# Performance work log

Hardware: AMD Instinct MI355X
Metric: run time of the kernel (lower is better)

The kernel has to match this reference:

```python
import jax, jax.numpy as jnp
import numpy as np

UNITS = 32      # 12 inter + 19 command + 1 motor
SENSORY = 32    # dense_2 output dim
MOTOR = 1
ODE_UNFOLDS = 6
EPS = 1e-8


def _build_wiring():
    # kerasncp NCP wiring: motor ids [0,1), command [1,20), inter [20,32)
    rng = np.random.RandomState(42)
    inter = np.arange(20, 32)
    command = np.arange(1, 20)
    motor = np.arange(0, 1)
    adj = np.zeros((UNITS, UNITS), np.float32)
    sens = np.zeros((SENSORY, UNITS), np.float32)
    for s in range(SENSORY):                      # sensory_fanout=6 onto inter neurons
        for d in rng.choice(inter, 6, replace=False):
            sens[s, d] = rng.choice([-1.0, 1.0])
    for i in inter:                               # inter_fanout=4 onto command neurons
        for d in rng.choice(command, 4, replace=False):
            adj[i, d] = rng.choice([-1.0, 1.0])
    for _ in range(6):                            # 6 recurrent command synapses
        adj[rng.choice(command), rng.choice(command)] = rng.choice([-1.0, 1.0])
    for m in motor:                               # motor_fanin=4 from command neurons
        for srcn in rng.choice(command, 4, replace=False):
            adj[srcn, m] = rng.choice([-1.0, 1.0])
    return adj, sens


def setup_inputs() -> dict:
    key = jax.random.key(0)
    ks = jax.random.split(key, 12)
    B, T = 256, 1024
    adj, sens = _build_wiring()
    u = lambda k, sh, lo, hi: jax.random.uniform(k, sh, jnp.float32, lo, hi)
    return {
        "x": jax.random.normal(ks[0], (B, T, 2), jnp.float32),
        "d1_w": jax.random.normal(ks[1], (2, 128), jnp.float32) * (1.0 / np.sqrt(2.0)),
        "d1_b": jnp.zeros((128,), jnp.float32),
        "d2_w": jax.random.normal(ks[2], (128, SENSORY), jnp.float32) * (1.0 / np.sqrt(128.0)),
        "d2_b": jnp.zeros((SENSORY,), jnp.float32),
        "input_w": jnp.ones((SENSORY,), jnp.float32),
        "input_b": jnp.zeros((SENSORY,), jnp.float32),
        "output_w": jnp.ones((MOTOR,), jnp.float32),
        "output_b": jnp.zeros((MOTOR,), jnp.float32),
        "gleak": u(ks[3], (UNITS,), 0.001, 1.0),
        "vleak": u(ks[4], (UNITS,), -0.2, 0.2),
        "cm": u(ks[5], (UNITS,), 0.4, 0.6),
        "w_syn": u(ks[6], (UNITS, UNITS), 0.001, 1.0),
        "mu": u(ks[7], (UNITS, UNITS), 0.3, 0.8),
        "sigma": u(ks[8], (UNITS, UNITS), 3.0, 8.0),
        "erev": jnp.asarray(adj),
        "sensory_w": u(ks[9], (SENSORY, UNITS), 0.001, 1.0),
        "sensory_mu": u(ks[10], (SENSORY, UNITS), 0.3, 0.8),
        "sensory_sigma": u(ks[11], (SENSORY, UNITS), 3.0, 8.0),
        "sensory_erev": jnp.asarray(sens),
        "sparsity_mask": jnp.asarray(np.abs(adj), jnp.int32),
        "sensory_mask": jnp.asarray(np.abs(sens), jnp.int32),
    }


def reference(x, d1_w, d1_b, d2_w, d2_b, input_w, input_b, output_w, output_b,
              gleak, vleak, cm, w_syn, mu, sigma, erev,
              sensory_w, sensory_mu, sensory_sigma, sensory_erev,
              sparsity_mask, sensory_mask):
    # Dense stack (per timestep)
    h = jax.nn.relu(x @ d1_w + d1_b)          # [B,T,128]
    h = h @ d2_w + d2_b                        # [B,T,32] sensory inputs
    spm = sparsity_mask.astype(h.dtype)
    ssm = sensory_mask.astype(h.dtype)

    def gate(v, m, s):                         # v [B,pre] -> [B,pre,post]
        return jax.nn.sigmoid(s * (v[..., None] - m))

    cm_t = cm * ODE_UNFOLDS                    # cm / (elapsed_time / ode_unfolds), elapsed_time=1

    def step(v, xt):
        inp = xt * input_w + input_b           # LTC input mapping (affine)
        sa = sensory_w * gate(inp, sensory_mu, sensory_sigma) * ssm   # [B,32,32]
        wnum_s = jnp.sum(sa * sensory_erev, axis=1)                   # [B,32]
        wden_s = jnp.sum(sa, axis=1)

        def unfold(vp, _):
            wa = w_syn * gate(vp, mu, sigma) * spm                    # [B,32,32]
            wnum = jnp.sum(wa * erev, axis=1) + wnum_s
            wden = jnp.sum(wa, axis=1) + wden_s
            vp = (cm_t * vp + gleak * vleak + wnum) / (cm_t + gleak + wden + EPS)
            return vp, None

        v, _ = jax.lax.scan(unfold, v, None, length=ODE_UNFOLDS)
        return v, None

    v0 = jnp.zeros((h.shape[0], UNITS), h.dtype)
    vT, _ = jax.lax.scan(step, v0, jnp.swapaxes(h, 0, 1))  # scan over T
    # output mapping: motor neurons are the first MOTOR states
    return vT[:, :MOTOR] * output_w + output_b             # [B,1]
```

## Files before the change

kernel.cpp:

```cpp
#include <hip/hip_runtime.h>
#include <math.h>

#define NB 256
#define NT 1024
#define NUNF 6
#define TB 64
#define CHK 8
#define L2E 1.44269504088896340736f
#define PI_F 3.14159265358979324f

typedef const float* fp;

extern "C" __device__ float __ocml_exp2_f32(float);
__device__ __forceinline__ float frcp(float x) { return __builtin_amdgcn_rcpf(x); }
__device__ __forceinline__ float ex2(float x) { return __ocml_exp2_f32(x); }
__device__ __forceinline__ float sgm(float a, float b, float v) { return frcp(1.f + ex2(fmaf(a, v, b))); }

struct Tables {
    int ngroups, npos, nchunks, pad0;
    int grp_start[21];
    int ord[20];
    int pos[20];
    int aff[20];
    int need_traj[20];
    int ch_ps[20], ch_pe[20], ch_gs[20], ch_ge[20];
    int ncp[20], nip[20], ngp[20];
    float cmt[20], cn0[20], cd0[20];
    float icmt[12];
    int   cp_pre[20][8];
    float cp_a[20][8], cp_b[20][8], cp_w[20][8], cp_e[20][8];
    int   ip_i[20][12];
    float ip_a[20][12], ip_b[20][12], ip_w[20][12], ip_e[20][12];
    int   gp_pre[20][6];
    float gp_a[20][6], gp_b[20][6], gp_w[20][6], gp_e[20][6];
};

struct DenseTab {
    int cnt[12];
    float in0[12], id0[12];
    int   pre[12][32];
    float a[12][32], b[12][32], w[12][32], e[12][32];
    int homog, maxcnt;
};

#define WS_DTAB   16384
#define WS_BND    24576
#define WS_BMASK  25600
#define WS_MG     32768
#define WS_VST    98304
#define WS_SENSI  131072

__global__ void build_tables(fp wsyn, fp mu, fp sigma, fp erev, const int* spm,
                             fp sw, fp smu, fp ssg, fp serev, const int* smask,
                             fp cm, fp gleak, fp vleak, fp d1b, Tables* T, DenseTab* D) {
    __shared__ int   spmL[1024], smkL[1024];
    __shared__ float wL[1024], muL[1024], sgL[1024], evL[1024];
    __shared__ float swL[1024], smuL[1024], ssgL[1024], sevL[1024];
    __shared__ float cmL[32], glL[32], vlL[32];
    __shared__ int premaskL[20], ancL[20], rootL[20], depUL[20], keyL[20], posL[20], ordL[20];
    __shared__ int ngpL[20];
    __shared__ int neededS;
    __shared__ float habs[64];
    __shared__ int cntS[12];
    int tid = threadIdx.x;
    for (int k = tid; k < 1024; k += 64) {
        spmL[k] = spm[k]; wL[k] = wsyn[k]; muL[k] = mu[k]; sgL[k] = sigma[k]; evL[k] = erev[k];
        smkL[k] = smask[k]; swL[k] = sw[k]; smuL[k] = smu[k]; ssgL[k] = ssg[k]; sevL[k] = serev[k];
    }
    if (tid < 32) { cmL[tid] = cm[tid]; glL[tid] = gleak[tid]; vlL[tid] = vleak[tid]; }
    habs[tid] = fmaxf(fabsf(d1b[tid]), fabsf(d1b[tid + 64]));
    __syncthreads();
    if (tid < 20) {
        int pm = 0;
        for (int i = 0; i < 20; ++i) if (spmL[i * 32 + tid]) pm |= 1 << i;
        premaskL[tid] = pm;
        ancL[tid] = pm;
    }
    __syncthreads();
    for (int it = 0; it < 20; ++it) {
        int a = 0;
        if (tid < 20) {
            a = ancL[tid];
            int pm = premaskL[tid];
            for (int i = 0; i < 20; ++i) if ((pm >> i) & 1) a |= ancL[i];
        }
        __syncthreads();
        if (tid < 20) ancL[tid] = a;
        __syncthreads();
    }
    if (tid == 0) neededS = ancL[0] | 1;
    __syncthreads();
    int needed = neededS;
    if (tid < 20) {
        int r = tid;
        if ((needed >> tid) & 1) {
            int aj = ancL[tid];
            for (int i = 0; i < 20; ++i)
                if (i < r && ((needed >> i) & 1) && ((aj >> i) & 1) && ((ancL[i] >> tid) & 1)) r = i;
        }
        rootL[tid] = r;
        depUL[tid] = 0;
    }
    __syncthreads();
    for (int it = 0; it < 21; ++it) {
        int d = 0;
        if (tid < 20 && ((needed >> tid) & 1)) {
            int pm = premaskL[tid], myr = rootL[tid];
            for (int i = 0; i < 20; ++i)
                if (((pm >> i) & 1) && rootL[i] != myr) d = max(d, depUL[i] + 1);
        }
        __syncthreads();
        if (tid < 20 && d > depUL[tid]) depUL[tid] = d;
        __syncthreads();
    }
    if (tid < 20) {
        int key = 0x7FFFFFFF;
        if ((needed >> tid) & 1) {
            int myr = rootL[tid], dg = 0;
            for (int i = 0; i < 20; ++i)
                if (((needed >> i) & 1) && rootL[i] == myr) dg = max(dg, depUL[i]);
            key = dg * 32 + myr;
        }
        keyL[tid] = key;
    }
    __syncthreads();
    if (tid < 20) {
        int mykey = keyL[tid];
        int p = 0;
        for (int k = 0; k < 20; ++k)
            if (keyL[k] < mykey || (keyL[k] == mykey && k < tid)) ++p;
        posL[tid] = p;
        if (p < 20) ordL[p] = tid;
    }
    __syncthreads();
    if (tid < 20) {
        int j = tid, cc = 0, ci = 0, cg = 0;
        T->cmt[j] = cmL[j] * (float)NUNF;
        T->cn0[j] = glL[j] * vlL[j];
        T->cd0[j] = cmL[j] * (float)NUNF + glL[j] + 1e-8f;
        if ((needed >> j) & 1) {
            int myr = rootL[j];
            int mystart = posL[myr];
            for (int i = 0; i < 32; ++i) {
                int p = i * 32 + j;
                if (!spmL[p]) continue;
                float sg = sgL[p];
                float a = -sg * L2E, b = sg * muL[p] * L2E;
                float w = wL[p], e = w * evL[p];
                if (i >= 20) {
                    T->ip_i[j][ci] = i - 20;
                    T->ip_a[j][ci] = a; T->ip_b[j][ci] = b; T->ip_w[j][ci] = w; T->ip_e[j][ci] = e;
                    ++ci;
                } else if (rootL[i] == myr) {
                    T->gp_pre[j][cg] = posL[i] - mystart;
                    T->gp_a[j][cg] = a; T->gp_b[j][cg] = b; T->gp_w[j][cg] = w; T->gp_e[j][cg] = e;
                    ++cg;
                } else {
                    T->cp_pre[j][cc] = posL[i];
                    T->cp_a[j][cc] = a; T->cp_b[j][cc] = b; T->cp_w[j][cc] = w; T->cp_e[j][cc] = e;
                    ++cc;
                }
            }
        }
        T->ncp[j] = cc; T->nip[j] = ci; T->ngp[j] = cg;
        ngpL[j] = cg;
    }
    if (tid < 12) {
        T->icmt[tid] = cmL[20 + tid] * (float)NUNF;
        int unit = 20 + tid, cnt = 0;
        for (int s = 0; s < 32; ++s) {
            int p = s * 32 + unit;
            if (!smkL[p]) continue;
            float sg = ssgL[p];
            D->pre[tid][cnt] = s;
            D->a[tid][cnt] = -sg * L2E;
            D->b[tid][cnt] = sg * smuL[p] * L2E;
            D->w[tid][cnt] = swL[p];
            D->e[tid][cnt] = swL[p] * sevL[p];
            ++cnt;
        }
        for (int c = cnt; c < 32; ++c) {
            D->pre[tid][c] = 0; D->a[tid][c] = 0.f; D->b[tid][c] = 0.f;
            D->w[tid][c] = 0.f; D->e[tid][c] = 0.f;
        }
        D->cnt[tid] = cnt;
        cntS[tid] = cnt;
        D->in0[tid] = glL[unit] * vlL[unit];
        D->id0[tid] = cmL[unit] * (float)NUNF + glL[unit] + 1e-8f;
    }
    __syncthreads();
    if (tid == 0) {
        int npos = __popc(needed & 0xFFFFF);
        T->npos = npos;
        int ng = 0, prevkey = -1;
        for (int p = 0; p < npos; ++p) {
            int u = ordL[p];
            if (keyL[u] != prevkey) { T->grp_start[ng] = p; ++ng; prevkey = keyL[u]; }
        }
        T->ngroups = ng;
        for (int g = ng; g <= 20; ++g) T->grp_start[g] = npos;
        for (int p = 0; p < 20; ++p) T->ord[p] = (p < npos) ? ordL[p] : 0;
        for (int j = 0; j < 20; ++j) T->pos[j] = posL[j];
        for (int g = 0; g < ng; ++g) {
            int gs = T->grp_start[g], ge = T->grp_start[g + 1], gsz = ge - gs;
            for (int p = gs; p < ge; ++p)
                T->aff[p] = (gsz == 1 && ngpL[ordL[p]] == 0) ? 1 : 0;
        }
        for (int p = npos; p < 20; ++p) T->aff[p] = 0;
        for (int p = 0; p < 20; ++p) T->need_traj[p] = 0;
        for (int i = 0; i < 20; ++i) {
            if (!((needed >> i) & 1)) continue;
            for (int j = 0; j < 20; ++j)
                if (j != i && ((needed >> j) & 1) && spmL[i * 32 + j]) { T->need_traj[posL[i]] = 1; break; }
        }
        int nchunks = 0, g = 0;
        while (g < ng) {
            int lvl = keyL[ordL[T->grp_start[g]]] / 32;
            int ge = g;
            while (ge < ng && keyL[ordL[T->grp_start[ge]]] / 32 == lvl) ++ge;
            int cs = g;
            while (cs < ge) {
                int ce = cs, acc = 0;
                while (ce < ge) {
                    int gsz = T->grp_start[ce + 1] - T->grp_start[ce];
                    if (acc + gsz > CHK && ce > cs) break;
                    acc += gsz; ++ce;
                    if (acc >= CHK) break;
                }
                T->ch_gs[nchunks] = cs; T->ch_ge[nchunks] = ce;
                T->ch_ps[nchunks] = T->grp_start[cs]; T->ch_pe[nchunks] = T->grp_start[ce];
                ++nchunks;
                cs = ce;
            }
            g = ge;
        }
        T->nchunks = nchunks;
        float hm = 0.f;
        for (int k = 0; k < 64; ++k) hm = fmaxf(hm, habs[k]);
        D->homog = (hm == 0.f) ? 1 : 0;
        int mc = 0;
        for (int k = 0; k < 12; ++k) mc = max(mc, cntS[k]);
        D->maxcnt = mc;
    }
}

__global__ void sector_prep(fp d1w, float* bnd, int* bmask) {
    __shared__ float ang[256];
    __shared__ float uS[128], vS[128];
    int tid = threadIdx.x;
    if (tid < 128) { uS[tid] = d1w[tid]; vS[tid] = d1w[128 + tid]; }
    __syncthreads();
    {
        int k = tid & 127;
        float al = atan2f(vS[k], uS[k]);
        float bb = (tid < 128) ? al + 1.57079632679489662f : al - 1.57079632679489662f;
        if (bb > PI_F) bb -= 2.f * PI_F;
        if (bb <= -PI_F) bb += 2.f * PI_F;
        ang[tid] = bb;
    }
    __syncthreads();
    for (int k = 2; k <= 256; k <<= 1) {
        for (int j = k >> 1; j > 0; j >>= 1) {
            int ixj = tid ^ j;
            if (ixj > tid) {
                float a0 = ang[tid], a1 = ang[ixj];
                bool up = ((tid & k) == 0);
                if ((a0 > a1) == up) { ang[tid] = a1; ang[ixj] = a0; }
            }
            __syncthreads();
        }
    }
    bnd[tid] = ang[tid];
    float lo = ang[tid];
    float hi = (tid < 255) ? ang[tid + 1] : ang[0] + 2.f * PI_F;
    float tm = 0.5f * (lo + hi);
    float ct = cosf(tm), st = sinf(tm);
    for (int w = 0; w < 4; ++w) {
        int m = 0;
        for (int kk = 0; kk < 32; ++kk) {
            int k = w * 32 + kk;
            if (fmaf(uS[k], ct, vS[k] * st) > 0.f) m |= 1 << kk;
        }
        bmask[tid * 4 + w] = m;
    }
}

__global__ void sector_M(fp d1w, fp d2w, fp iw, const int* bmask, float2* Mg) {
    int s = blockIdx.x, j = threadIdx.x;
    if (j >= 32) return;
    float acc0 = 0.f, acc1 = 0.f;
#pragma unroll
    for (int w = 0; w < 4; ++w) {
        int mm = bmask[s * 4 + w];
        for (int kk = 0; kk < 32; ++kk) {
            if ((mm >> kk) & 1) {
                int k = w * 32 + kk;
                float w2 = d2w[k * 32 + j];
                acc0 = fmaf(d1w[k], w2, acc0);
                acc1 = fmaf(d1w[128 + k], w2, acc1);
            }
        }
    }
    float iwj = iw[j];
    Mg[s * 32 + j] = make_float2(acc0 * iwj, acc1 * iwj);
}

__global__ __launch_bounds__(256) void dense_homog(
    fp x, fp d2b, fp iw, fp ib,
    const DenseTab* __restrict__ Dg, const float2* __restrict__ Mg, const float* __restrict__ bndg,
    float2* sensI, int t0, int CT) {
    if (Dg->homog == 0) return;
    __shared__ float bndL[256];
    __shared__ float4 tabT[416];
    __shared__ int   preT[416];
    __shared__ float ibuf[4][2112];
    __shared__ float b2q[32], iwq[32], ibq[32];
    __shared__ float in0L[12], id0L[12];
    int tid = threadIdx.x;
    for (int idx = tid; idx < 384; idx += 256) {
        int d = idx >> 5, e = idx & 31;
        int sl = e * 13 + d;
        tabT[sl] = make_float4(Dg->a[d][e], Dg->b[d][e], Dg->w[d][e], Dg->e[d][e]);
        preT[sl] = Dg->pre[d][e];
    }
    if (tid < 12) { in0L[tid] = Dg->in0[tid]; id0L[tid] = Dg->id0[tid]; }
    if (tid < 32) { b2q[tid] = d2b[tid]; iwq[tid] = iw[tid]; ibq[tid] = ib[tid]; }
    if (tid < 256) bndL[tid] = bndg[tid];
    __syncthreads();
    int wid = tid >> 6, lane = tid & 63;
    const float2* x2 = (const float2*)x;
    int gw = blockIdx.x * 4 + wid;
    int nw = gridDim.x * 4;
    float* ibf = ibuf[wid];
    int jj = lane & 31, h = lane >> 5;
    float cj = fmaf(b2q[jj], iwq[jj], ibq[jj]);
    int cntmax = Dg->maxcnt;
    int pass_total = (NB * CT) >> 6;
    for (int pass = gw; pass < pass_total; pass += nw) {
        int cg0 = pass * 64;
        int cg = cg0 + lane;
        int lt = cg >> 8, bb_ = cg & 255;
        float2 xv = x2[bb_ * NT + (t0 + lt)];
        float th = atan2f(xv.y, xv.x);
        int sec;
        if (th < bndL[0]) sec = 255;
        else {
            int lo = 0, hi = 255;
#pragma unroll
            for (int it7 = 0; it7 < 8; ++it7) {
                int mid = (lo + hi + 1) >> 1;
                if (bndL[mid] <= th) lo = mid; else hi = mid - 1;
            }
            sec = lo;
        }
        float x0r = xv.x, x1r = xv.y;
#pragma unroll 4
        for (int r = 0; r < 32; ++r) {
            int item = 2 * r + h;
            int s_it = __shfl(sec, item);
            float xi0 = __shfl(x0r, item);
            float xi1 = __shfl(x1r, item);
            float2 m = Mg[s_it * 32 + jj];
            ibf[item * 33 + jj] = fmaf(xi0, m.x, fmaf(xi1, m.y, cj));
        }
        __builtin_amdgcn_wave_barrier();
#pragma unroll
        for (int rb = 0; rb < 12; ++rb) {
            int task = rb * 64 + lane;
            int item = task / 12;
            int dd = task - item * 12;
            float wn = in0L[dd], wd = id0L[dd];
            for (int e = 0; e < cntmax; ++e) {
                int sl = e * 13 + dd;
                float4 tb = tabT[sl];
                float pv = ibf[item * 33 + preT[sl]];
                float gq = frcp(1.f + ex2(fmaf(tb.x, pv, tb.y)));
                wn = fmaf(tb.w, gq, wn);
                wd = fmaf(tb.z, gq, wd);
            }
            int cg2 = cg0 + item;
            int lt2 = cg2 >> 8, b2_ = cg2 & 255;
            sensI[(size_t)(b2_ * CT + lt2) * 12 + dd] = make_float2(wn, wd);
        }
        __builtin_amdgcn_wave_barrier();
    }
}

__global__ __launch_bounds__(256) void dense_general(
    fp x, fp d1w, fp d1b, fp d2w, fp d2b, fp iw, fp ib,
    const DenseTab* __restrict__ Dg, float2* sensI, int t0, int CT) {
    if (Dg->homog != 0) return;
    __shared__ float W2s[4096];
    __shared__ float W1s[256], b1s[128];
    __shared__ float b2q[32], iwq[32], ibq[32];
    __shared__ float4 tabT[416];
    __shared__ int   preT[416];
    __shared__ int   cntL[12];
    __shared__ float in0L[12], id0L[12];
    __shared__ float hbuf[4][128][20];
    __shared__ float ibuf[4][16][33];
    int tid = threadIdx.x;
    for (int idx = tid; idx < 384; idx += 256) {
        int d = idx >> 5, e = idx & 31;
        int sl = e * 13 + d;
        tabT[sl] = make_float4(Dg->a[d][e], Dg->b[d][e], Dg->w[d][e], Dg->e[d][e]);
        preT[sl] = Dg->pre[d][e];
    }
    if (tid < 12) { cntL[tid] = Dg->cnt[tid]; in0L[tid] = Dg->in0[tid]; id0L[tid] = Dg->id0[tid]; }
    for (int p = tid; p < 4096; p += 256) W2s[p] = d2w[p];
    if (tid < 256) W1s[tid] = d1w[tid];
    if (tid < 128) b1s[tid] = d1b[tid];
    if (tid < 32) { b2q[tid] = d2b[tid]; iwq[tid] = iw[tid]; ibq[tid] = ib[tid]; }
    __syncthreads();
    int wid = tid >> 6, lane = tid & 63;
    float* hb = (float*)hbuf[wid];
    float* ibf = (float*)ibuf[wid];
    const float2* x2 = (const float2*)x;
    int gw = blockIdx.x * 4 + wid;
    int nw = gridDim.x * 4;
    int pass_total = (NB * CT) >> 4;
    int itd1 = lane >> 2, kq = lane & 3;
    int j = lane & 31, half = lane >> 5;
    for (int pass = gw; pass < pass_total; pass += nw) {
        int cg0 = pass * 16;
        {
            int cg = cg0 + itd1;
            int lt = cg >> 8, b = cg & 255;
            float2 xv = x2[b * NT + (t0 + lt)];
#pragma unroll 8
            for (int i = 0; i < 32; ++i) {
                int k = kq + 4 * i;
                float hk = fmaf(xv.y, W1s[128 + k], fmaf(xv.x, W1s[k], b1s[k]));
                hb[k * 20 + itd1] = hk > 0.f ? hk : 0.f;
            }
        }
        __builtin_amdgcn_wave_barrier();
        {
            float a0=0,a1=0,a2=0,a3=0,a4=0,a5=0,a6=0,a7=0;
#pragma unroll 4
            for (int k = 0; k < 128; ++k) {
                float w2 = W2s[k * 32 + j];
                float4 ha = *(const float4*)&hb[k * 20 + half * 8];
                float4 hbv = *(const float4*)&hb[k * 20 + half * 8 + 4];
                a0 = fmaf(ha.x, w2, a0); a1 = fmaf(ha.y, w2, a1);
                a2 = fmaf(ha.z, w2, a2); a3 = fmaf(ha.w, w2, a3);
                a4 = fmaf(hbv.x, w2, a4); a5 = fmaf(hbv.y, w2, a5);
                a6 = fmaf(hbv.z, w2, a6); a7 = fmaf(hbv.w, w2, a7);
            }
            float bb = b2q[j], iww = iwq[j], ibb = ibq[j];
            ibf[(half*8+0)*33+j] = fmaf(a0+bb, iww, ibb);
            ibf[(half*8+1)*33+j] = fmaf(a1+bb, iww, ibb);
            ibf[(half*8+2)*33+j] = fmaf(a2+bb, iww, ibb);
            ibf[(half*8+3)*33+j] = fmaf(a3+bb, iww, ibb);
            ibf[(half*8+4)*33+j] = fmaf(a4+bb, iww, ibb);
            ibf[(half*8+5)*33+j] = fmaf(a5+bb, iww, ibb);
            ibf[(half*8+6)*33+j] = fmaf(a6+bb, iww, ibb);
            ibf[(half*8+7)*33+j] = fmaf(a7+bb, iww, ibb);
        }
        __builtin_amdgcn_wave_barrier();
#pragma unroll
        for (int r = 0; r < 3; ++r) {
            int task = r * 64 + lane;
            int it = task / 12;
            int d = task - it * 12;
            int cnt = cntL[d];
            float wn = in0L[d], wd = id0L[d];
            for (int e = 0; e < cnt; ++e) {
                int sl = e * 13 + d;
                float4 tb = tabT[sl];
                float gq = frcp(1.f + ex2(fmaf(tb.x, ibf[it * 33 + preT[sl]], tb.y)));
                wn = fmaf(tb.w, gq, wn);
                wd = fmaf(tb.z, gq, wd);
            }
            int cg = cg0 + it;
            int lt = cg >> 8, b = cg & 255;
            sensI[(size_t)(b * CT + lt) * 12 + d] = make_float2(wn, wd);
        }
        __builtin_amdgcn_wave_barrier();
    }
}

__global__ __launch_bounds__(512) void solve(const float2* __restrict__ sensI,
                                             const Tables* __restrict__ Tg,
                                             fp ow, fp ob, float* vstate,
                                             int t0, int CT, float* out) {
    __shared__ Tables TL;
    __shared__ float2 iAB[TB * 12];
    __shared__ float2 icomp[TB * 12];
    __shared__ float viter[TB * 13];
    __shared__ float vtraj[20 * TB * 7];
    __shared__ float2 pnpd[CHK * TB * 7];
    __shared__ float2 comp[CHK * TB];
    __shared__ float vstart[CHK * TB];
    __shared__ float gstate[20], istate[12];
    int tid = threadIdx.x;
    int b = blockIdx.x;
    {
        const int nw = (int)(sizeof(Tables) / 4);
        const int* src = (const int*)Tg;
        int* dst = (int*)&TL;
        for (int k = tid; k < nw; k += 512) dst[k] = src[k];
    }
    __syncthreads();
    if (tid < 20 && tid < TL.npos)
        gstate[tid] = (t0 == 0) ? 0.f : vstate[b * 32 + TL.ord[tid]];
    if (tid < 12)
        istate[tid] = (t0 == 0) ? 0.f : vstate[b * 32 + 20 + tid];
    __syncthreads();
    int ntiles = CT / TB;
    bool lastChunk = (t0 + CT == NT);
    for (int tile = 0; tile < ntiles; ++tile) {
        int tbase = tile * TB;
        for (int w = tid; w < TB * 16; w += 512) {
            int tt = w >> 4, ii = w & 15;
            if (ii < 12) {
                float2 s = sensI[(size_t)(b * CT + tbase + tt) * 12 + ii];
                float r = frcp(s.y);
                float A = TL.icmt[ii] * r, B = s.x * r;
                iAB[tt * 12 + ii] = make_float2(A, B);
                float A2 = A * A, A4 = A2 * A2;
                float A6 = A4 * A2;
                float B6 = B * (1.f + A) * (1.f + A2 + A4);
                icomp[tt * 12 + ii] = make_float2(A6, B6);
            }
        }
        __syncthreads();
        if (tid < 12) {
            float v = istate[tid];
#pragma unroll 4
            for (int tt = 0; tt < TB; ++tt) {
                viter[tt * 13 + tid] = v;
                float2 cc = icomp[tt * 12 + tid];
                v = fmaf(cc.x, v, cc.y);
            }
            istate[tid] = v;
        }
        __syncthreads();
        int nchunks = TL.nchunks;
        for (int c = 0; c < nchunks; ++c) {
            int ps = TL.ch_ps[c], pe = TL.ch_pe[c];
            int gs0 = TL.ch_gs[c], ge0 = TL.ch_ge[c];
            int npc = pe - ps;
            for (int w = tid; w < npc * TB; w += 512) {
                int m = w >> 6, tt = w & (TB - 1);
                int posi = ps + m;
                int unit = TL.ord[posi];
                float pn[6], pd[6];
#pragma unroll
                for (int u = 0; u < 6; ++u) { pn[u] = TL.cn0[unit]; pd[u] = TL.cd0[unit]; }
                int ncp = TL.ncp[unit];
                for (int e = 0; e < ncp; ++e) {
                    int pp = TL.cp_pre[unit][e];
                    float a = TL.cp_a[unit][e], bb = TL.cp_b[unit][e];
                    float w_ = TL.cp_w[unit][e], ev = TL.cp_e[unit][e];
#pragma unroll
                    for (int u = 0; u < 6; ++u) {
                        float gq = sgm(a, bb, vtraj[(pp * TB + tt) * 7 + u]);
                        pn[u] = fmaf(ev, gq, pn[u]);
                        pd[u] = fmaf(w_, gq, pd[u]);
                    }
                }
                int nip = TL.nip[unit];
                for (int e = 0; e < nip; ++e) {
                    int ii = TL.ip_i[unit][e];
                    float2 ab = iAB[tt * 12 + ii];
                    float vi = viter[tt * 13 + ii];
                    float a = TL.ip_a[unit][e], bb = TL.ip_b[unit][e];
                    float w_ = TL.ip_w[unit][e], ev = TL.ip_e[unit][e];
#pragma unroll
                    for (int u = 0; u < 6; ++u) {
                        float gq = sgm(a, bb, vi);
                        pn[u] = fmaf(ev, gq, pn[u]);
                        pd[u] = fmaf(w_, gq, pd[u]);
                        vi = fmaf(ab.x, vi, ab.y);
                    }
                }
                if (TL.aff[posi]) {
                    float cmt = TL.cmt[unit];
                    float Ac = 1.f, Bc = 0.f;
#pragma unroll
                    for (int u = 0; u < 6; ++u) {
                        float r = frcp(pd[u]);
                        float Au = cmt * r, Bu = pn[u] * r;
                        pnpd[(m * TB + tt) * 7 + u] = make_float2(Au, Bu);
                        Bc = fmaf(Au, Bc, Bu);
                        Ac *= Au;
                    }
                    comp[m * TB + tt] = make_float2(Ac, Bc);
                } else {
#pragma unroll
                    for (int u = 0; u < 6; ++u)
                        pnpd[(m * TB + tt) * 7 + u] = make_float2(pn[u], pd[u]);
                }
            }
            __syncthreads();
            if (tid < ge0 - gs0) {
                int g = gs0 + tid;
                int gs = TL.grp_start[g], ge = TL.grp_start[g + 1], gsz = ge - gs;
                int m0 = gs - ps;
                if (gsz == 1) {
                    int unit = TL.ord[gs];
                    float v = gstate[gs];
                    if (TL.aff[gs]) {
#pragma unroll 4
                        for (int tt = 0; tt < TB; ++tt) {
                            vstart[m0 * TB + tt] = v;
                            float2 cc = comp[m0 * TB + tt];
                            v = fmaf(cc.x, v, cc.y);
                        }
                    } else {
                        float ga = TL.gp_a[unit][0], gb = TL.gp_b[unit][0];
                        float gw = TL.gp_w[unit][0], gev = TL.gp_e[unit][0];
                        float cmt = TL.cmt[unit];
                        int ntj = TL.need_traj[gs];
                        for (int tt = 0; tt < TB; ++tt) {
#pragma unroll
                            for (int u = 0; u < 6; ++u) {
                                if (ntj) vtraj[(gs * TB + tt) * 7 + u] = v;
                                float2 pp2 = pnpd[(m0 * TB + tt) * 7 + u];
                                float E = ex2(fmaf(ga, v, gb));
                                float P = fmaf(cmt, v, pp2.x);
                                float N = fmaf(P, E, P + gev);
                                float Dd = fmaf(pp2.y, E, pp2.y + gw);
                                v = N * frcp(Dd);
                            }
                        }
                    }
                    gstate[gs] = v;
                } else {
                    float sv[CHK], nv[CHK];
#pragma unroll
                    for (int mm = 0; mm < CHK; ++mm) if (mm < gsz) sv[mm] = gstate[gs + mm];
                    for (int tt = 0; tt < TB; ++tt) {
#pragma unroll
                        for (int u = 0; u < 6; ++u) {
#pragma unroll
                            for (int mm = 0; mm < CHK; ++mm)
                                if (mm < gsz) vtraj[((gs + mm) * TB + tt) * 7 + u] = sv[mm];
#pragma unroll
                            for (int mm = 0; mm < CHK; ++mm) {
                                if (mm < gsz) {
                                    int unit = TL.ord[gs + mm];
                                    float2 pp2 = pnpd[((m0 + mm) * TB + tt) * 7 + u];
                                    float wn = pp2.x, wd = pp2.y;
                                    int ngpu = TL.ngp[unit];
#pragma unroll
                                    for (int e = 0; e < 6; ++e) {
                                        if (e < ngpu) {
                                            float vp = sv[TL.gp_pre[unit][e]];
                                            float gq = sgm(TL.gp_a[unit][e], TL.gp_b[unit][e], vp);
                                            wn = fmaf(TL.gp_e[unit][e], gq, wn);
                                            wd = fmaf(TL.gp_w[unit][e], gq, wd);
                                        }
                                    }
                                    nv[mm] = fmaf(TL.cmt[unit], sv[mm], wn) * frcp(wd);
                                }
                            }
#pragma unroll
                            for (int mm = 0; mm < CHK; ++mm) if (mm < gsz) sv[mm] = nv[mm];
                        }
                    }
#pragma unroll
                    for (int mm = 0; mm < CHK; ++mm) if (mm < gsz) gstate[gs + mm] = sv[mm];
                }
            }
            __syncthreads();
            for (int w = tid; w < npc * TB; w += 512) {
                int m = w >> 6, tt = w & (TB - 1);
                int posi = ps + m;
                if (TL.aff[posi] && TL.need_traj[posi]) {
                    float v = vstart[m * TB + tt];
#pragma unroll
                    for (int u = 0; u < 6; ++u) {
                        vtraj[(posi * TB + tt) * 7 + u] = v;
                        float2 ab = pnpd[(m * TB + tt) * 7 + u];
                        v = fmaf(ab.x, v, ab.y);
                    }
                }
            }
            __syncthreads();
        }
    }
    if (tid < 20 && tid < TL.npos) vstate[b * 32 + TL.ord[tid]] = gstate[tid];
    if (tid < 12) vstate[b * 32 + 20 + tid] = istate[tid];
    if (lastChunk) {
        __syncthreads();
        if (tid == 0) out[b] = fmaf(gstate[TL.pos[0]], ow[0], ob[0]);
    }
}

extern "C" void kernel_launch(void* const* d_in, const int* in_sizes, int n_in,
                              void* d_out, int out_size, void* d_ws, size_t ws_size,
                              hipStream_t stream) {
    fp x     = (fp)d_in[0];
    fp d1w   = (fp)d_in[1];
    fp d1b   = (fp)d_in[2];
    fp d2w   = (fp)d_in[3];
    fp d2b   = (fp)d_in[4];
    fp iw    = (fp)d_in[5];
    fp ib    = (fp)d_in[6];
    fp ow    = (fp)d_in[7];
    fp ob    = (fp)d_in[8];
    fp gleak = (fp)d_in[9];
    fp vleak = (fp)d_in[10];
    fp cm    = (fp)d_in[11];
    fp wsyn  = (fp)d_in[12];
    fp mu    = (fp)d_in[13];
    fp sigma = (fp)d_in[14];
    fp erev  = (fp)d_in[15];
    fp sw    = (fp)d_in[16];
    fp smu   = (fp)d_in[17];
    fp ssg   = (fp)d_in[18];
    fp serev = (fp)d_in[19];
    const int* spm   = (const int*)d_in[20];
    const int* smask = (const int*)d_in[21];

    char* wsb = (char*)d_ws;
    Tables*   T = (Tables*)wsb;
    DenseTab* D = (DenseTab*)(wsb + WS_DTAB);
    float*   bnd = (float*)(wsb + WS_BND);
    int*   bmask = (int*)(wsb + WS_BMASK);
    float2*   Mg = (float2*)(wsb + WS_MG);
    float* vstate = (float*)(wsb + WS_VST);
    float2* sensI = (float2*)(wsb + WS_SENSI);

    size_t per_t = (size_t)NB * 12 * sizeof(float2);
    int CT = TB;
    if (ws_size > WS_SENSI) {
        size_t m = (ws_size - WS_SENSI) / per_t;
        int ct = TB;
        while (ct < NT && (size_t)(ct * 2) <= m) ct *= 2;
        CT = ct;
    }

    build_tables<<<1, 64, 0, stream>>>(wsyn, mu, sigma, erev, spm,
                                       sw, smu, ssg, serev, smask,
                                       cm, gleak, vleak, d1b, T, D);
    sector_prep<<<1, 256, 0, stream>>>(d1w, bnd, bmask);
    sector_M<<<256, 64, 0, stream>>>(d1w, d2w, iw, bmask, Mg);

    int nch = NT / CT;
    for (int c = 0; c < nch; ++c) {
        int t0 = c * CT;
        dense_homog<<<768, 256, 0, stream>>>(x, d2b, iw, ib, D, Mg, bnd, sensI, t0, CT);
        dense_general<<<512, 256, 0, stream>>>(x, d1w, d1b, d2w, d2b, iw, ib, D, sensI, t0, CT);
        solve<<<NB, 512, 0, stream>>>(sensI, T, ow, ob, vstate, t0, CT, (float*)d_out);
    }
}
```

Measured before the change: 298.1 us.

## Double solve time tile via compacted trajectory slots and on-the-fly inter compose

Doubles the solve kernel's time tile from 64 to 128 steps, which halves the number of tile iterations and their barriers per block. To fit in shared memory, trajectory storage is compacted so only command neurons that feed others get a slot, with indices remapped in the tables. The precomputed icomp buffer is removed and the inter-neuron sixth-power composition is now computed inside the serial 12-thread loop. The larger shared footprint may reduce occupancy, and the serial inter loop does more arithmetic per step.

```diff
diff --git a/kernel.cpp b/kernel.cpp
--- a/kernel.cpp
+++ b/kernel.cpp
@@ -4,8 +4,9 @@
 #define NB 256
 #define NT 1024
 #define NUNF 6
-#define TB 64
+#define TBS 128
 #define CHK 8
+#define NTJMAX 12
 #define L2E 1.44269504088896340736f
 #define PI_F 3.14159265358979324f
 
@@ -17,12 +18,13 @@
 __device__ __forceinline__ float sgm(float a, float b, float v) { return frcp(1.f + ex2(fmaf(a, v, b))); }
 
 struct Tables {
-    int ngroups, npos, nchunks, pad0;
+    int ngroups, npos, nchunks, ntraj;
     int grp_start[21];
     int ord[20];
     int pos[20];
     int aff[20];
     int need_traj[20];
+    int traj_slot[20];
     int ch_ps[20], ch_pe[20], ch_gs[20], ch_ge[20];
     int ncp[20], nip[20], ngp[20];
     float cmt[20], cn0[20], cd0[20];
@@ -58,7 +60,7 @@
     __shared__ float swL[1024], smuL[1024], ssgL[1024], sevL[1024];
     __shared__ float cmL[32], glL[32], vlL[32];
     __shared__ int premaskL[20], ancL[20], rootL[20], depUL[20], keyL[20], posL[20], ordL[20];
-    __shared__ int ngpL[20];
+    __shared__ int ngpL[20], ntjL[20], slotU[20];
     __shared__ int neededS;
     __shared__ float habs[64];
     __shared__ int cntS[12];
@@ -131,6 +133,20 @@
             if (keyL[k] < mykey || (keyL[k] == mykey && k < tid)) ++p;
         posL[tid] = p;
         if (p < 20) ordL[p] = tid;
+    }
+    __syncthreads();
+    if (tid < 20) {
+        int nt = 0;
+        if ((needed >> tid) & 1)
+            for (int j = 0; j < 20; ++j)
+                if (j != tid && ((needed >> j) & 1) && spmL[tid * 32 + j]) { nt = 1; break; }
+        ntjL[tid] = nt;
+    }
+    __syncthreads();
+    if (tid == 0) {
+        int s = 0;
+        for (int p = 0; p < 20; ++p) { int u = ordL[p]; slotU[u] = s; s += ntjL[u]; }
+        T->ntraj = s;
     }
     __syncthreads();
     if (tid < 20) {
@@ -156,7 +172,7 @@
                     T->gp_a[j][cg] = a; T->gp_b[j][cg] = b; T->gp_w[j][cg] = w; T->gp_e[j][cg] = e;
                     ++cg;
                 } else {
-                    T->cp_pre[j][cc] = posL[i];
+                    T->cp_pre[j][cc] = slotU[i];
                     T->cp_a[j][cc] = a; T->cp_b[j][cc] = b; T->cp_w[j][cc] = w; T->cp_e[j][cc] = e;
                     ++cc;
                 }
@@ -207,11 +223,10 @@
                 T->aff[p] = (gsz == 1 && ngpL[ordL[p]] == 0) ? 1 : 0;
         }
         for (int p = npos; p < 20; ++p) T->aff[p] = 0;
-        for (int p = 0; p < 20; ++p) T->need_traj[p] = 0;
-        for (int i = 0; i < 20; ++i) {
-            if (!((needed >> i) & 1)) continue;
-            for (int j = 0; j < 20; ++j)
-                if (j != i && ((needed >> j) & 1) && spmL[i * 32 + j]) { T->need_traj[posL[i]] = 1; break; }
+        for (int p = 0; p < 20; ++p) {
+            int u = ordL[p];
+            T->need_traj[p] = ntjL[u];
+            T->traj_slot[p] = slotU[u];
         }
         int nchunks = 0, g = 0;
         while (g < ng) {
@@ -485,13 +500,12 @@
                                              fp ow, fp ob, float* vstate,
                                              int t0, int CT, float* out) {
     __shared__ Tables TL;
-    __shared__ float2 iAB[TB * 12];
-    __shared__ float2 icomp[TB * 12];
-    __shared__ float viter[TB * 13];
-    __shared__ float vtraj[20 * TB * 7];
-    __shared__ float2 pnpd[CHK * TB * 7];
-    __shared__ float2 comp[CHK * TB];
-    __shared__ float vstart[CHK * TB];
+    __shared__ float2 iAB[TBS * 12];
+    __shared__ float viter[TBS * 13];
+    __shared__ float vtraj[NTJMAX * TBS * 7];
+    __shared__ float2 pnpd[CHK * TBS * 7];
+    __shared__ float2 comp[CHK * TBS];
+    __shared__ float vstart[CHK * TBS];
     __shared__ float gstate[20], istate[12];
     int tid = threadIdx.x;
     int b = blockIdx.x;
@@ -507,31 +521,30 @@
     if (tid < 12)
         istate[tid] = (t0 == 0) ? 0.f : vstate[b * 32 + 20 + tid];
     __syncthreads();
-    int ntiles = CT / TB;
+    int ntiles = CT / TBS;
     bool lastChunk = (t0 + CT == NT);
     for (int tile = 0; tile < ntiles; ++tile) {
-        int tbase = tile * TB;
-        for (int w = tid; w < TB * 16; w += 512) {
+        int tbase = tile * TBS;
+        for (int w = tid; w < TBS * 16; w += 512) {
             int tt = w >> 4, ii = w & 15;
             if (ii < 12) {
                 float2 s = sensI[(size_t)(b * CT + tbase + tt) * 12 + ii];
                 float r = frcp(s.y);
-                float A = TL.icmt[ii] * r, B = s.x * r;
-                iAB[tt * 12 + ii] = make_float2(A, B);
-                float A2 = A * A, A4 = A2 * A2;
-                float A6 = A4 * A2;
-                float B6 = B * (1.f + A) * (1.f + A2 + A4);
-                icomp[tt * 12 + ii] = make_float2(A6, B6);
+                iAB[tt * 12 + ii] = make_float2(TL.icmt[ii] * r, s.x * r);
             }
         }
         __syncthreads();
         if (tid < 12) {
             float v = istate[tid];
 #pragma unroll 4
-            for (int tt = 0; tt < TB; ++tt) {
+            for (int tt = 0; tt < TBS; ++tt) {
+                float2 ab = iAB[tt * 12 + tid];
+                float A = ab.x, B = ab.y;
+                float A2 = A * A, A4 = A2 * A2;
+                float A6 = A4 * A2;
+                float B6 = B * (1.f + A) * (1.f + A2 + A4);
                 viter[tt * 13 + tid] = v;
-                float2 cc = icomp[tt * 12 + tid];
-                v = fmaf(cc.x, v, cc.y);
+                v = fmaf(A6, v, B6);
             }
             istate[tid] = v;
         }
@@ -541,8 +554,8 @@
             int ps = TL.ch_ps[c], pe = TL.ch_pe[c];
             int gs0 = TL.ch_gs[c], ge0 = TL.ch_ge[c];
             int npc = pe - ps;
-            for (int w = tid; w < npc * TB; w += 512) {
-                int m = w >> 6, tt = w & (TB - 1);
+            for (int w = tid; w < npc * TBS; w += 512) {
+                int m = w >> 7, tt = w & (TBS - 1);
                 int posi = ps + m;
                 int unit = TL.ord[posi];
                 float pn[6], pd[6];
@@ -550,12 +563,12 @@
                 for (int u = 0; u < 6; ++u) { pn[u] = TL.cn0[unit]; pd[u] = TL.cd0[unit]; }
                 int ncp = TL.ncp[unit];
                 for (int e = 0; e < ncp; ++e) {
-                    int pp = TL.cp_pre[unit][e];
+                    int sl = TL.cp_pre[unit][e];
                     float a = TL.cp_a[unit][e], bb = TL.cp_b[unit][e];
                     float w_ = TL.cp_w[unit][e], ev = TL.cp_e[unit][e];
 #pragma unroll
                     for (int u = 0; u < 6; ++u) {
-                        float gq = sgm(a, bb, vtraj[(pp * TB + tt) * 7 + u]);
+                        float gq = sgm(a, bb, vtraj[(sl * TBS + tt) * 7 + u]);
                         pn[u] = fmaf(ev, gq, pn[u]);
                         pd[u] = fmaf(w_, gq, pd[u]);
                     }
@@ -582,15 +595,15 @@
                     for (int u = 0; u < 6; ++u) {
                         float r = frcp(pd[u]);
                         float Au = cmt * r, Bu = pn[u] * r;
-                        pnpd[(m * TB + tt) * 7 + u] = make_float2(Au, Bu);
+                        pnpd[(m * TBS + tt) * 7 + u] = make_float2(Au, Bu);
                         Bc = fmaf(Au, Bc, Bu);
                         Ac *= Au;
                     }
-                    comp[m * TB + tt] = make_float2(Ac, Bc);
+                    comp[m * TBS + tt] = make_float2(Ac, Bc);
                 } else {
 #pragma unroll
                     for (int u = 0; u < 6; ++u)
-                        pnpd[(m * TB + tt) * 7 + u] = make_float2(pn[u], pd[u]);
+                        pnpd[(m * TBS + tt) * 7 + u] = make_float2(pn[u], pd[u]);
                 }
             }
             __syncthreads();
@@ -603,9 +616,9 @@
                     float v = gstate[gs];
                     if (TL.aff[gs]) {
 #pragma unroll 4
-                        for (int tt = 0; tt < TB; ++tt) {
-                            vstart[m0 * TB + tt] = v;
-                            float2 cc = comp[m0 * TB + tt];
+                        for (int tt = 0; tt < TBS; ++tt) {
+                            vstart[m0 * TBS + tt] = v;
+                            float2 cc = comp[m0 * TBS + tt];
                             v = fmaf(cc.x, v, cc.y);
                         }
                     } else {
@@ -613,11 +626,12 @@
                         float gw = TL.gp_w[unit][0], gev = TL.gp_e[unit][0];
                         float cmt = TL.cmt[unit];
                         int ntj = TL.need_traj[gs];
-                        for (int tt = 0; tt < TB; ++tt) {
+                        int sl = TL.traj_slot[gs];
+                        for (int tt = 0; tt < TBS; ++tt) {
 #pragma unroll
                             for (int u = 0; u < 6; ++u) {
-                                if (ntj) vtraj[(gs * TB + tt) * 7 + u] = v;
-                                float2 pp2 = pnpd[(m0 * TB + tt) * 7 + u];
+                                if (ntj) vtraj[(sl * TBS + tt) * 7 + u] = v;
+                                float2 pp2 = pnpd[(m0 * TBS + tt) * 7 + u];
                                 float E = ex2(fmaf(ga, v, gb));
                                 float P = fmaf(cmt, v, pp2.x);
                                 float N = fmaf(P, E, P + gev);
@@ -631,17 +645,18 @@
                     float sv[CHK], nv[CHK];
 #pragma unroll
                     for (int mm = 0; mm < CHK; ++mm) if (mm < gsz) sv[mm] = gstate[gs + mm];
-                    for (int tt = 0; tt < TB; ++tt) {
+                    for (int tt = 0; tt < TBS; ++tt) {
 #pragma unroll
                         for (int u = 0; u < 6; ++u) {
 #pragma unroll
                             for (int mm = 0; mm < CHK; ++mm)
-                                if (mm < gsz) vtraj[((gs + mm) * TB + tt) * 7 + u] = sv[mm];
+                                if (mm < gsz && TL.need_traj[gs + mm])
+                                    vtraj[(TL.traj_slot[gs + mm] * TBS + tt) * 7 + u] = sv[mm];
 #pragma unroll
                             for (int mm = 0; mm < CHK; ++mm) {
                                 if (mm < gsz) {
                                     int unit = TL.ord[gs + mm];
-                                    float2 pp2 = pnpd[((m0 + mm) * TB + tt) * 7 + u];
+                                    float2 pp2 = pnpd[((m0 + mm) * TBS + tt) * 7 + u];
                                     float wn = pp2.x, wd = pp2.y;
                                     int ngpu = TL.ngp[unit];
 #pragma unroll
@@ -665,15 +680,16 @@
                 }
             }
             __syncthreads();
-            for (int w = tid; w < npc * TB; w += 512) {
-                int m = w >> 6, tt = w & (TB - 1);
+            for (int w = tid; w < npc * TBS; w += 512) {
+                int m = w >> 7, tt = w & (TBS - 1);
                 int posi = ps + m;
                 if (TL.aff[posi] && TL.need_traj[posi]) {
-                    float v = vstart[m * TB + tt];
+                    int sl = TL.traj_slot[posi];
+                    float v = vstart[m * TBS + tt];
 #pragma unroll
                     for (int u = 0; u < 6; ++u) {
-                        vtraj[(posi * TB + tt) * 7 + u] = v;
-                        float2 ab = pnpd[(m * TB + tt) * 7 + u];
+                        vtraj[(sl * TBS + tt) * 7 + u] = v;
+                        float2 ab = pnpd[(m * TBS + tt) * 7 + u];
                         v = fmaf(ab.x, v, ab.y);
                     }
                 }
@@ -725,10 +741,10 @@
     float2* sensI = (float2*)(wsb + WS_SENSI);
 
     size_t per_t = (size_t)NB * 12 * sizeof(float2);
-    int CT = TB;
+    int CT = TBS;
     if (ws_size > WS_SENSI) {
         size_t m = (ws_size - WS_SENSI) / per_t;
-        int ct = TB;
+        int ct = TBS;
         while (ct < NT && (size_t)(ct * 2) <= m) ct *= 2;
         CT = ct;
     }
```

After: 276.0 us. 7.4% less time.
